# Performance work log

Hardware: AMD Instinct MI355X
Metric: run time of the kernel (lower is better)

## Reference

```python
import jax, jax.numpy as jnp
import numpy as np

B = 16384      # rays
H = 128        # field hidden dim


def setup_inputs() -> dict:
    key = jax.random.key(0)
    ks = jax.random.split(key, 8)
    origins = jax.random.normal(ks[0], (B, 3), dtype=jnp.float32)
    directions = jax.random.normal(ks[1], (B, 3), dtype=jnp.float32)
    directions = directions / jnp.linalg.norm(directions, axis=-1, keepdims=True)
    # Field: simple MLP 3 -> H -> H -> 4 (rgb + sigma)
    W1 = jax.random.normal(ks[2], (3, H), dtype=jnp.float32) * (1.0 / np.sqrt(3.0))
    b1 = jnp.zeros((H,), dtype=jnp.float32)
    W2 = jax.random.normal(ks[3], (H, H), dtype=jnp.float32) * (1.0 / np.sqrt(H))
    b2 = jnp.zeros((H,), dtype=jnp.float32)
    W3 = jax.random.normal(ks[4], (H, 4), dtype=jnp.float32) * (1.0 / np.sqrt(H))
    b3 = jnp.zeros((4,), dtype=jnp.float32)
    return {"origins": origins, "directions": directions,
            "W1": W1, "b1": b1, "W2": W2, "b2": b2, "W3": W3, "b3": b3,
            "near": 2, "far": 6, "num_samples": 64}


def _field(x, W1, b1, W2, b2, W3, b3):
    h = jax.nn.relu(x @ W1 + b1)
    h = jax.nn.relu(h @ W2 + b2)
    return h @ W3 + b3


def reference(origins, directions, W1, b1, W2, b2, W3, b3, near, far, num_samples):
    near = jnp.float32(near)
    far = jnp.float32(far)
    # 1. generate_samples: segment boundaries + midpoints along each ray
    depths = jnp.linspace(near, far, num_samples + 1)            # [S+1]
    midpoints = 0.5 * (depths[:-1] + depths[1:])                 # [S]
    # [B, S, 3] = origin + t * direction
    locs = origins[:, None, :] + midpoints[None, :, None] * directions[:, None, :]
    # 2. evaluate field
    f = _field(locs.reshape(-1, 3), W1, b1, W2, b2, W3, b3)
    f = f.reshape(origins.shape[0], num_samples, 4)
    # NOTE: source overwrites the sigmoid'd colors with raw outputs (faithful)
    colors = f[..., :3]                                          # [B, S, 3]
    sigma = f[..., 3]                                            # [B, S]
    # 3. alpha values
    delta = depths[1:] - depths[:-1]                             # [S]
    alphas = 1.0 - jnp.exp(-sigma * delta[None, :])              # [B, S]
    # 4. alpha compositing (black background)
    ones = jnp.ones_like(alphas[:, :1])
    transmittance = jnp.cumprod(jnp.concatenate([ones, 1.0 - alphas], axis=1), axis=1)[:, :-1]
    weights = alphas * transmittance                             # [B, S]
    radiance = jnp.sum(weights[..., None] * colors, axis=1)      # [B, 3]
    return radiance
```

## Files before the change

kernel.cpp:

```cpp
#include <hip/hip_runtime.h>


typedef _Float16 f16;
typedef __attribute__((ext_vector_type(2))) _Float16 h2v;
typedef __attribute__((ext_vector_type(8))) _Float16 half8;
typedef __attribute__((ext_vector_type(4))) float floatx4;

#define H 128
#define NS 64
#define A_STRIDE 136

static __device__ __forceinline__ h2v pkrtz(float a, float b) {
  return __builtin_bit_cast(h2v, __builtin_amdgcn_cvt_pkrtz(a, b));
}

__global__ void nerf_setup(const float* __restrict__ W2, const float* __restrict__ W3,
                           const float* __restrict__ b2,
                           f16* __restrict__ wsW2, f16* __restrict__ wsW3,
                           f16* __restrict__ wsB2) {
  int t = blockIdx.x * blockDim.x + threadIdx.x;
  if (t < 8192) {
    int j2 = t & 3, lane = (t >> 2) & 63, mt = (t >> 8) & 7, ks = t >> 11;
    int k = ks * 32 + ((lane >> 4) * 8) + 2 * j2;
    int n = mt * 16 + (lane & 15);
    wsW2[2 * t]     = (f16)W2[k * H + n];
    wsW2[2 * t + 1] = (f16)W2[(k + 1) * H + n];
  } else if (t < 9216) {
    int u = t - 8192;
    int j2 = u & 3, lane = (u >> 2) & 63, ks = u >> 8;
    int k = ks * 32 + ((lane >> 4) * 8) + 2 * j2;
    int c = lane & 15;
    wsW3[2 * u]     = (c < 4) ? (f16)W3[k * 4 + c]       : (f16)0.0f;
    wsW3[2 * u + 1] = (c < 4) ? (f16)W3[(k + 1) * 4 + c] : (f16)0.0f;
  } else if (t < 9344) {
    int i = t - 9216;
    int b32i = i >> 1, e = i & 1;
    int quad = b32i >> 4, rem = b32i & 15, mt = rem >> 1, p = rem & 1;
    wsB2[i] = (f16)b2[mt * 16 + quad * 4 + 2 * p + e];
  }
}

__global__ __launch_bounds__(256, 2) void nerf_main(
    const float* __restrict__ origins, const float* __restrict__ dirs,
    const float* __restrict__ W1, const float* __restrict__ b1,
    const float* __restrict__ b3,
    const f16* __restrict__ wsW2, const f16* __restrict__ wsW3,
    const f16* __restrict__ wsB2,
    float* __restrict__ out)
{
  __shared__ __align__(16) f16   a_lds[256][A_STRIDE];
  __shared__ __align__(16) f16   popd[4][2][H];
  __shared__ __align__(16) float f_lds[4][64][4];

  const int t = threadIdx.x;
  const int w = t >> 6, lane = t & 63, quad = lane >> 4, l16 = lane & 15;
  const int prow0 = w * 64;
  const float delta = 4.0f / NS;
  const int ray = blockIdx.x * 4 + w;

  {
    const float o0 = origins[ray*3], o1 = origins[ray*3+1], o2 = origins[ray*3+2];
    const float d0 = dirs[ray*3],    d1 = dirs[ray*3+1],    d2 = dirs[ray*3+2];
    const int k0 = lane * 2;
    const float2 wr0 = *(const float2*)&W1[0*H + k0];
    const float2 wr1 = *(const float2*)&W1[1*H + k0];
    const float2 wr2 = *(const float2*)&W1[2*H + k0];
    const float2 bb  = *(const float2*)&b1[k0];
    float poa = fmaf(o2, wr2.x, fmaf(o1, wr1.x, fmaf(o0, wr0.x, bb.x)));
    float pob = fmaf(o2, wr2.y, fmaf(o1, wr1.y, fmaf(o0, wr0.y, bb.y)));
    float pda = fmaf(d2, wr2.x, fmaf(d1, wr1.x, d0 * wr0.x));
    float pdb = fmaf(d2, wr2.y, fmaf(d1, wr1.y, d0 * wr0.y));
    h2v po2; po2[0] = (f16)poa; po2[1] = (f16)pob;
    h2v pd2; pd2[0] = (f16)pda; pd2[1] = (f16)pdb;
    *(h2v*)&popd[w][0][k0] = po2;
    *(h2v*)&popd[w][1][k0] = pd2;
  }

  half8 m8[4];
  #pragma unroll
  for (int tr = 0; tr < 4; ++tr)
    m8[tr] = (half8)(f16)(2.0f + (tr*16 + l16 + 0.5f) * delta);

  floatx4 acc[8][4];
  #pragma unroll
  for (int mt = 0; mt < 8; ++mt)
    #pragma unroll
    for (int tr = 0; tr < 4; ++tr) acc[mt][tr] = (floatx4)(0.0f);

  const half8* w2f = (const half8*)wsW2;
  const half8 z8 = (half8)(f16)0.0f;
  half8 awA[8], awB[8];
  #pragma unroll
  for (int mt = 0; mt < 8; ++mt) awA[mt] = w2f[mt*64 + lane];

  #pragma unroll
  for (int ks = 0; ks < 4; ++ks) {
    half8* cur = (ks & 1) ? awB : awA;
    half8* nxt = (ks & 1) ? awA : awB;
    if (ks < 3) {
      #pragma unroll
      for (int mt = 0; mt < 8; ++mt) nxt[mt] = w2f[((ks+1)*8 + mt)*64 + lane];
    }
    const half8 po8 = *(const half8*)&popd[w][0][ks*32 + quad*8];
    const half8 pd8 = *(const half8*)&popd[w][1][ks*32 + quad*8];
    #pragma unroll
    for (int tr = 0; tr < 4; ++tr) {
      half8 hb = pd8 * m8[tr] + po8;
      hb = __builtin_elementwise_max(hb, z8);
      #pragma unroll
      for (int mt = 0; mt < 8; ++mt)
        acc[mt][tr] = __builtin_amdgcn_mfma_f32_16x16x32_f16(cur[mt], hb, acc[mt][tr], 0, 0, 0);
    }
  }

  h2v bpk[8][2];
  {
    const uint2* bp = (const uint2*)wsB2;
    #pragma unroll
    for (int mt = 0; mt < 8; ++mt) {
      union { uint2 u; h2v h[2]; } pk;
      pk.u = bp[quad * 8 + mt];
      bpk[mt][0] = pk.h[0]; bpk[mt][1] = pk.h[1];
    }
  }
  const h2v z2 = (h2v)(f16)0.0f;
  #pragma unroll
  for (int mt = 0; mt < 8; ++mt)
    #pragma unroll
    for (int tr = 0; tr < 4; ++tr) {
      h2v c0 = pkrtz(acc[mt][tr][0], acc[mt][tr][1]);
      h2v c1 = pkrtz(acc[mt][tr][2], acc[mt][tr][3]);
      c0 = __builtin_elementwise_max((h2v)(c0 + bpk[mt][0]), z2);
      c1 = __builtin_elementwise_max((h2v)(c1 + bpk[mt][1]), z2);
      union { h2v h[2]; uint2 u; } pk; pk.h[0] = c0; pk.h[1] = c1;
      *(uint2*)&a_lds[prow0 + tr*16 + l16][mt*16 + quad*4] = pk.u;
    }

  floatx4 acc3[4];
  #pragma unroll
  for (int tr = 0; tr < 4; ++tr) acc3[tr] = (floatx4)(0.0f);
  const half8* w3f = (const half8*)wsW3;
  half8 w3[4];
  #pragma unroll
  for (int ks = 0; ks < 4; ++ks) w3[ks] = w3f[ks*64 + lane];
  #pragma unroll
  for (int tr = 0; tr < 4; ++tr)
    #pragma unroll
    for (int ks = 0; ks < 4; ++ks) {
      const half8 a = *(const half8*)&a_lds[prow0 + tr*16 + l16][ks*32 + quad*8];
      acc3[tr] = __builtin_amdgcn_mfma_f32_16x16x32_f16(a, w3[ks], acc3[tr], 0, 0, 0);
    }
  if (l16 < 4) {
    const float bc = b3[l16];
    #pragma unroll
    for (int tr = 0; tr < 4; ++tr)
      #pragma unroll
      for (int r = 0; r < 4; ++r)
        f_lds[w][tr*16 + quad*4 + r][l16] = acc3[tr][r] + bc;
  }

  {
    const float4 fv = *(const float4*)&f_lds[w][lane][0];
    const float sigma = fv.w;
    const float alpha = 1.0f - __expf(-sigma * delta);
    float S = sigma;
    #pragma unroll
    for (int off = 1; off < 64; off <<= 1) {
      float u = __shfl_up(S, off);
      if (lane >= off) S += u;
    }
    const float T  = __expf(-delta * (S - sigma));
    const float wt = alpha * T;
    float cr = wt * fv.x, cg = wt * fv.y, cb = wt * fv.z;
    #pragma unroll
    for (int off = 32; off > 0; off >>= 1) {
      cr += __shfl_down(cr, off);
      cg += __shfl_down(cg, off);
      cb += __shfl_down(cb, off);
    }
    if (lane == 0) {
      out[ray*3+0] = cr; out[ray*3+1] = cg; out[ray*3+2] = cb;
    }
  }
}

extern "C" void kernel_launch(void* const* d_in, const int* in_sizes, int n_in,
                              void* d_out, int out_size, void* d_ws, size_t ws_size,
                              hipStream_t stream) {
  const float* origins = (const float*)d_in[0];
  const float* dirs    = (const float*)d_in[1];
  const float* W1      = (const float*)d_in[2];
  const float* b1      = (const float*)d_in[3];
  const float* W2      = (const float*)d_in[4];
  const float* b2      = (const float*)d_in[5];
  const float* W3      = (const float*)d_in[6];
  const float* b3      = (const float*)d_in[7];
  float* out = (float*)d_out;

  f16* wsW2 = (f16*)d_ws;
  f16* wsW3 = wsW2 + 16384;
  f16* wsB2 = wsW3 + 2048;

  nerf_setup<<<37, 256, 0, stream>>>(W2, W3, b2, wsW2, wsW3, wsB2);
  nerf_main<<<16384 / 4, 256, 0, stream>>>(
      origins, dirs, W1, b1, b3, wsW2, wsW3, wsB2, out);
}
```

Baseline: 111.7 us.

## Keep layer-2 activations in registers by permuting W2/W3 layouts, drop LDS staging

Permutes the prepacked W2 columns and W3 rows so the layer-2 MFMA output fragments can feed the layer-3 MFMA directly as the B operand, which removes the 256x136 f16 LDS staging buffer and its write/read round trip. The layer-3 MFMA is transposed (W3 as A), so output channels land in register slots and quad 0 writes float4 rows to f_lds. Freeing about 70KB of LDS lets launch bounds rise to 4 blocks per CU, trading register pressure (hpk holds 64 packed values) for higher occupancy.

```diff
diff --git a/kernel.cpp b/kernel.cpp
--- a/kernel.cpp
+++ b/kernel.cpp
@@ -8,7 +8,6 @@
 
 #define H 128
 #define NS 64
-#define A_STRIDE 136
 
 static __device__ __forceinline__ h2v pkrtz(float a, float b) {
   return __builtin_bit_cast(h2v, __builtin_amdgcn_cvt_pkrtz(a, b));
@@ -21,26 +20,25 @@
   int t = blockIdx.x * blockDim.x + threadIdx.x;
   if (t < 8192) {
     int j2 = t & 3, lane = (t >> 2) & 63, mt = (t >> 8) & 7, ks = t >> 11;
+    int l16 = lane & 15;
     int k = ks * 32 + ((lane >> 4) * 8) + 2 * j2;
-    int n = mt * 16 + (lane & 15);
+    int n = 32 * (l16 >> 2) + mt * 4 + (l16 & 3);
     wsW2[2 * t]     = (f16)W2[k * H + n];
     wsW2[2 * t + 1] = (f16)W2[(k + 1) * H + n];
   } else if (t < 9216) {
     int u = t - 8192;
     int j2 = u & 3, lane = (u >> 2) & 63, ks = u >> 8;
-    int k = ks * 32 + ((lane >> 4) * 8) + 2 * j2;
     int c = lane & 15;
-    wsW3[2 * u]     = (c < 4) ? (f16)W3[k * 4 + c]       : (f16)0.0f;
-    wsW3[2 * u + 1] = (c < 4) ? (f16)W3[(k + 1) * 4 + c] : (f16)0.0f;
+    int k3 = 32 * (lane >> 4) + ks * 8 + 2 * j2;
+    wsW3[2 * u]     = (c < 4) ? (f16)W3[k3 * 4 + c]       : (f16)0.0f;
+    wsW3[2 * u + 1] = (c < 4) ? (f16)W3[(k3 + 1) * 4 + c] : (f16)0.0f;
   } else if (t < 9344) {
     int i = t - 9216;
-    int b32i = i >> 1, e = i & 1;
-    int quad = b32i >> 4, rem = b32i & 15, mt = rem >> 1, p = rem & 1;
-    wsB2[i] = (f16)b2[mt * 16 + quad * 4 + 2 * p + e];
-  }
-}
-
-__global__ __launch_bounds__(256, 2) void nerf_main(
+    wsB2[i] = (f16)b2[i];
+  }
+}
+
+__global__ __launch_bounds__(256, 4) void nerf_main(
     const float* __restrict__ origins, const float* __restrict__ dirs,
     const float* __restrict__ W1, const float* __restrict__ b1,
     const float* __restrict__ b3,
@@ -48,13 +46,11 @@
     const f16* __restrict__ wsB2,
     float* __restrict__ out)
 {
-  __shared__ __align__(16) f16   a_lds[256][A_STRIDE];
   __shared__ __align__(16) f16   popd[4][2][H];
   __shared__ __align__(16) float f_lds[4][64][4];
 
   const int t = threadIdx.x;
   const int w = t >> 6, lane = t & 63, quad = lane >> 4, l16 = lane & 15;
-  const int prow0 = w * 64;
   const float delta = 4.0f / NS;
   const int ray = blockIdx.x * 4 + w;
 
@@ -113,50 +109,51 @@
     }
   }
 
-  h2v bpk[8][2];
+  h2v hpk[8][4][2];
   {
     const uint2* bp = (const uint2*)wsB2;
+    const h2v z2 = (h2v)(f16)0.0f;
     #pragma unroll
     for (int mt = 0; mt < 8; ++mt) {
-      union { uint2 u; h2v h[2]; } pk;
-      pk.u = bp[quad * 8 + mt];
-      bpk[mt][0] = pk.h[0]; bpk[mt][1] = pk.h[1];
-    }
-  }
-  const h2v z2 = (h2v)(f16)0.0f;
-  #pragma unroll
-  for (int mt = 0; mt < 8; ++mt)
-    #pragma unroll
-    for (int tr = 0; tr < 4; ++tr) {
-      h2v c0 = pkrtz(acc[mt][tr][0], acc[mt][tr][1]);
-      h2v c1 = pkrtz(acc[mt][tr][2], acc[mt][tr][3]);
-      c0 = __builtin_elementwise_max((h2v)(c0 + bpk[mt][0]), z2);
-      c1 = __builtin_elementwise_max((h2v)(c1 + bpk[mt][1]), z2);
-      union { h2v h[2]; uint2 u; } pk; pk.h[0] = c0; pk.h[1] = c1;
-      *(uint2*)&a_lds[prow0 + tr*16 + l16][mt*16 + quad*4] = pk.u;
-    }
-
-  floatx4 acc3[4];
-  #pragma unroll
-  for (int tr = 0; tr < 4; ++tr) acc3[tr] = (floatx4)(0.0f);
+      union { uint2 u; h2v h[2]; } bk;
+      bk.u = bp[quad * 8 + mt];
+      #pragma unroll
+      for (int tr = 0; tr < 4; ++tr) {
+        h2v c0 = pkrtz(acc[mt][tr][0], acc[mt][tr][1]);
+        h2v c1 = pkrtz(acc[mt][tr][2], acc[mt][tr][3]);
+        hpk[mt][tr][0] = __builtin_elementwise_max((h2v)(c0 + bk.h[0]), z2);
+        hpk[mt][tr][1] = __builtin_elementwise_max((h2v)(c1 + bk.h[1]), z2);
+      }
+    }
+  }
+
   const half8* w3f = (const half8*)wsW3;
   half8 w3[4];
   #pragma unroll
   for (int ks = 0; ks < 4; ++ks) w3[ks] = w3f[ks*64 + lane];
+  floatx4 acc3[4];
+  #pragma unroll
+  for (int tr = 0; tr < 4; ++tr) acc3[tr] = (floatx4)(0.0f);
   #pragma unroll
   for (int tr = 0; tr < 4; ++tr)
     #pragma unroll
     for (int ks = 0; ks < 4; ++ks) {
-      const half8 a = *(const half8*)&a_lds[prow0 + tr*16 + l16][ks*32 + quad*8];
-      acc3[tr] = __builtin_amdgcn_mfma_f32_16x16x32_f16(a, w3[ks], acc3[tr], 0, 0, 0);
-    }
-  if (l16 < 4) {
-    const float bc = b3[l16];
-    #pragma unroll
-    for (int tr = 0; tr < 4; ++tr)
-      #pragma unroll
-      for (int r = 0; r < 4; ++r)
-        f_lds[w][tr*16 + quad*4 + r][l16] = acc3[tr][r] + bc;
+      union { h2v h[4]; half8 v; } b;
+      b.h[0] = hpk[2*ks][tr][0];   b.h[1] = hpk[2*ks][tr][1];
+      b.h[2] = hpk[2*ks+1][tr][0]; b.h[3] = hpk[2*ks+1][tr][1];
+      acc3[tr] = __builtin_amdgcn_mfma_f32_16x16x32_f16(w3[ks], b.v, acc3[tr], 0, 0, 0);
+    }
+
+  if (quad == 0) {
+    #pragma unroll
+    for (int tr = 0; tr < 4; ++tr) {
+      float4 fv;
+      fv.x = acc3[tr][0] + b3[0];
+      fv.y = acc3[tr][1] + b3[1];
+      fv.z = acc3[tr][2] + b3[2];
+      fv.w = acc3[tr][3] + b3[3];
+      *(float4*)&f_lds[w][tr*16 + l16][0] = fv;
+    }
   }
 
   {
```

New measurement: 335.0 us. 3x slower.
